# Performance work log

Hardware: AMD Instinct MI355X
Metric: run time of the kernel (lower is better)

The kernel has to match this reference:

```python
import jax, jax.numpy as jnp
import numpy as np

B, CIN, C, N, K = 2, 64, 128, 8192, 16
GROUPS = C // 16
EPS = 1e-5


def lrelu(x):
    return jnp.where(x >= 0, x, 0.1 * x)


def conv1d(x, w, b):  # x:(B,Ci,N) w:(Co,Ci)
    return jnp.einsum('oc,bcn->bon', w, x) + b[None, :, None]


def conv2d(x, w, b):  # x:(B,Ci,N,K) w:(Co,Ci)
    return jnp.einsum('oc,bcnk->bonk', w, x) + b[None, :, None, None]


def groupnorm(x, gamma, beta, groups=GROUPS):
    # normalize over (C/groups, *spatial) per sample per group
    b, c = x.shape[0], x.shape[1]
    xr = x.reshape(b, groups, -1)
    mean = xr.mean(-1, keepdims=True)
    var = xr.var(-1, keepdims=True)
    xn = ((xr - mean) * jax.lax.rsqrt(var + EPS)).reshape(x.shape)
    shp = (1, c) + (1,) * (x.ndim - 2)
    return xn * gamma.reshape(shp) + beta.reshape(shp)


def knn_idx(xyz, k):  # xyz:(B,3,N) -> idx:(B,N,K)
    pts = jnp.transpose(xyz, (0, 2, 1))  # (B,N,3)
    sq = jnp.sum(pts * pts, axis=-1)  # (B,N)
    inner = jnp.einsum('bnc,bmc->bnm', pts, pts)
    d2 = sq[:, :, None] + sq[:, None, :] - 2.0 * inner  # (B,N,N)
    _, idx = jax.lax.top_k(-d2, k)
    return idx


def group(x, idx):  # x:(B,C,N) idx:(B,N,K) -> (B,C,N,K)
    b, c, n = x.shape
    k = idx.shape[-1]
    idxe = jnp.broadcast_to(idx.reshape(b, 1, n * k), (b, c, n * k))
    return jnp.take_along_axis(x, idxe, axis=2).reshape(b, c, n, k)


def reference(xyz, feat, pre_w, pre_b, wq_w, wq_b, wk_w, wk_b, wv_w, wv_b,
              pos1_w, pos1_b, pos1_g, pos1_be, pos2_w, pos2_b,
              att1_w, att1_b, att1_g, att1_be, att2_w, att2_b,
              post_w, post_b, post_g, post_be):
    idx = knn_idx(xyz, K)  # (B,N,K)
    new_feat = conv1d(feat, pre_w, pre_b)  # (B,C,N)
    rel = group(xyz, idx) - xyz[:, :, :, None]  # (B,3,N,K)
    pos = lrelu(groupnorm(conv2d(rel, pos1_w, pos1_b), pos1_g, pos1_be))
    pos = conv2d(pos, pos2_w, pos2_b)  # (B,C,N,K)
    q = conv1d(new_feat, wq_w, wq_b)
    k = group(conv1d(new_feat, wk_w, wk_b), idx)  # (B,C,N,K)
    v = group(conv1d(new_feat, wv_w, wv_b), idx)
    att = q[:, :, :, None] - k + pos
    att = lrelu(groupnorm(conv2d(att, att1_w, att1_b), att1_g, att1_be))
    att = conv2d(att, att2_w, att2_b)
    att = jax.nn.softmax(att, axis=3)
    out = jnp.sum(att * v, axis=3)  # (B,C,N)
    out = lrelu(groupnorm(conv1d(out + new_feat, post_w, post_b), post_g, post_be))
    return out


def setup_inputs():
    key = jax.random.key(0)
    ks = jax.random.split(key, 16)
    s = 0.05
    d = {
        'xyz': jax.random.normal(ks[0], (B, 3, N), jnp.float32),
        'feat': jax.random.normal(ks[1], (B, CIN, N), jnp.float32),
        'pre_w': jax.random.normal(ks[2], (C, CIN), jnp.float32) * s,
        'pre_b': jnp.zeros((C,), jnp.float32),
        'wq_w': jax.random.normal(ks[3], (C, C), jnp.float32) * s,
        'wq_b': jnp.zeros((C,), jnp.float32),
        'wk_w': jax.random.normal(ks[4], (C, C), jnp.float32) * s,
        'wk_b': jnp.zeros((C,), jnp.float32),
        'wv_w': jax.random.normal(ks[5], (C, C), jnp.float32) * s,
        'wv_b': jnp.zeros((C,), jnp.float32),
        'pos1_w': jax.random.normal(ks[6], (C, 3), jnp.float32) * s,
        'pos1_b': jnp.zeros((C,), jnp.float32),
        'pos1_g': jnp.ones((C,), jnp.float32),
        'pos1_be': jnp.zeros((C,), jnp.float32),
        'pos2_w': jax.random.normal(ks[7], (C, C), jnp.float32) * s,
        'pos2_b': jnp.zeros((C,), jnp.float32),
        'att1_w': jax.random.normal(ks[8], (C, C), jnp.float32) * s,
        'att1_b': jnp.zeros((C,), jnp.float32),
        'att1_g': jnp.ones((C,), jnp.float32),
        'att1_be': jnp.zeros((C,), jnp.float32),
        'att2_w': jax.random.normal(ks[9], (C, C), jnp.float32) * s,
        'att2_b': jnp.zeros((C,), jnp.float32),
        'post_w': jax.random.normal(ks[10], (C, C), jnp.float32) * s,
        'post_b': jnp.zeros((C,), jnp.float32),
        'post_g': jnp.ones((C,), jnp.float32),
        'post_be': jnp.zeros((C,), jnp.float32),
    }
    return d
```

## Files before the change

### kernel.cpp

```cpp
#include <hip/hip_runtime.h>
#include <hip/hip_bf16.h>

#define BB 2
#define NN 8192
#define CC 128
#define CIN_ 64
#define KK 16
#define EPSV 1e-5f

typedef __attribute__((ext_vector_type(8))) short short8;
typedef __attribute__((ext_vector_type(4))) float f32x4;

static const size_t OFF_NF   = 262144;
static const size_t OFF_OUT2 = OFF_NF  + 2097152;
static const size_t OFF_Y    = OFF_OUT2 + 2097152;
static const size_t OFF_AQB  = OFF_Y   + 16777216;
static const size_t OFF_AKB  = OFF_AQB + 1048576;
static const size_t OFF_VFB  = OFF_AKB + 1048576;
static const size_t OFF_WQ2  = OFF_VFB + 1048576;
static const size_t OFF_WK2  = OFF_WQ2 + 16384;
static const size_t OFF_PWT  = OFF_WK2 + 16384;
static const size_t OFF_W2B  = OFF_PWT + 16384;
static const size_t OFF_A2B  = OFF_W2B + 8192;
static const size_t OFF_BY   = OFF_A2B + 8192;
static const size_t OFF_RST  = OFF_BY  + 128;
static const size_t OFF_REDA = OFF_RST + 32;
static const size_t OFF_REDP = OFF_REDA + 32;
static const size_t OFF_S1   = OFF_REDP + 32;
static const size_t OFF_T1   = OFF_S1 + 256;
static const size_t OFF_S2   = OFF_T1 + 256;
static const size_t OFF_T2   = OFF_S2 + 256;
static const size_t OFF_S3   = OFF_T2 + 256;
static const size_t OFF_T3   = OFF_S3 + 256;
static const size_t OFF_PTS4 = OFF_T3 + 256;
static const size_t OFF_PTA  = OFF_PTS4 + 65536;
static const size_t OFF_PTP  = OFF_PTA + 65536;

__device__ __forceinline__ unsigned fkey_u(float d) {
  unsigned u = __float_as_uint(d);
  return (u & 0x80000000u) ? ~u : (u | 0x80000000u);
}
__device__ __forceinline__ unsigned long long shflx64(unsigned long long v, int m) {
  int lo = __shfl_xor((int)(unsigned)(v & 0xffffffffu), m, 64);
  int hi = __shfl_xor((int)(unsigned)(v >> 32), m, 64);
  return ((unsigned long long)(unsigned)hi << 32) | (unsigned)lo;
}
__device__ __forceinline__ float bf2f(unsigned short u) {
  return __uint_as_float((unsigned)u << 16);
}
__device__ __forceinline__ unsigned short f2bf(float f) {
  __hip_bfloat16 h = __float2bfloat16(f);
  unsigned short r;
  __builtin_memcpy(&r, &h, 2);
  return r;
}
__device__ __forceinline__ unsigned pack2bf(float a, float b) {
  return (unsigned)f2bf(a) | ((unsigned)f2bf(b) << 16);
}

__global__ __launch_bounds__(128) void prep_weights(
    const float* __restrict__ att1_w, const float* __restrict__ wq_w, const float* __restrict__ wk_w,
    const float* __restrict__ pos2_w, const float* __restrict__ att2_w, const float* __restrict__ post_w,
    const float* __restrict__ wq_b, const float* __restrict__ wk_b, const float* __restrict__ pos2_b,
    const float* __restrict__ att1_b,
    float* __restrict__ WQ2, float* __restrict__ WK2, __hip_bfloat16* __restrict__ W2b,
    __hip_bfloat16* __restrict__ A2b, float* __restrict__ PWT, float* __restrict__ bias_y) {
  int blk = blockIdx.x, t = threadIdx.x;
  if (blk < 128) {
    int c = blk;
    __shared__ float row[128];
    row[t] = att1_w[c * 128 + t];
    __syncthreads();
    float sq = 0.f, sk = 0.f, sp = 0.f;
    for (int m = 0; m < 128; ++m) {
      float r = row[m];
      sq = fmaf(r, wq_w[m * 128 + t], sq);
      sk = fmaf(r, wk_w[m * 128 + t], sk);
      sp = fmaf(r, pos2_w[m * 128 + t], sp);
    }
    WQ2[c * 128 + t] = sq;
    WK2[c * 128 + t] = sk;
    W2b[c * 128 + t] = __float2bfloat16(sp);
  } else if (blk == 128) {
    for (int e = t; e < 16384; e += 128) {
      int c = e >> 7, cp = e & 127;
      A2b[e] = __float2bfloat16(att2_w[e]);
      PWT[cp * 128 + c] = post_w[e];
    }
  } else {
    float s = att1_b[t];
    for (int m = 0; m < 128; ++m)
      s = fmaf(att1_w[t * 128 + m], wq_b[m] - wk_b[m] + pos2_b[m], s);
    bias_y[t] = s;
  }
}

__global__ __launch_bounds__(256) void pts4_kernel(const float* __restrict__ xyz,
                                                   float4* __restrict__ pts4) {
  int e = blockIdx.x * 256 + threadIdx.x;
  int b = e >> 13, n = e & 8191;
  const float* X = xyz + b * 3 * NN;
  float x = X[n], y = X[NN + n], z = X[2 * NN + n];
  pts4[e] = make_float4(-2.0f * x, -2.0f * y, -2.0f * z, fmaf(z, z, fmaf(y, y, x * x)));
}

#define SLOTS 96
__global__ __launch_bounds__(512) void knn_kernel(const float4* __restrict__ pts4,
                                                  int* __restrict__ idxb) {
  __shared__ float4 tile[2048];
  __shared__ unsigned long long list[32][SLOTS];
  __shared__ float chm[32][33];
  __shared__ int cnt[32];
  int t = threadIdx.x;
  int wid = t >> 6, lane = t & 63;
  int q = lane & 31, sub = lane >> 5;
  int blk = blockIdx.x;
  int b = blk >> 8;
  int q0 = (blk & 255) << 5;
  const float4* P = pts4 + b * NN;
  float4 qv = P[q0 + q];
  float qx = -0.5f * qv.x, qy = -0.5f * qv.y, qz = -0.5f * qv.z;
  if (t < 32) cnt[t] = 0;
  int tbase = (wid << 8) + (sub << 7);

  {
    float4 r0 = P[t], r1 = P[512 + t], r2 = P[1024 + t], r3 = P[1536 + t];
    tile[t] = r0; tile[512 + t] = r1; tile[1024 + t] = r2; tile[1536 + t] = r3;
  }
  __syncthreads();
  for (int s = 0; s < 4; ++s) {
    float4 p0, p1, p2, p3;
    if (s < 3) {
      const float4* S = P + ((s + 1) << 11);
      p0 = S[t]; p1 = S[512 + t]; p2 = S[1024 + t]; p3 = S[1536 + t];
    }
    const float4* T = &tile[tbase];
    float mm = 3.4e38f;
    for (int i = 0; i < 128; i += 8) {
      float d[8];
#pragma unroll
      for (int u = 0; u < 8; ++u) {
        float4 cv = T[i + u];
        d[u] = fmaf(qx, cv.x, fmaf(qy, cv.y, fmaf(qz, cv.z, cv.w)));
      }
      mm = fminf(mm, fminf(fminf(fminf(d[0], d[1]), fminf(d[2], d[3])),
                           fminf(fminf(d[4], d[5]), fminf(d[6], d[7]))));
    }
    mm = fminf(mm, __shfl_xor(mm, 32));
    __syncthreads();
    if (s < 3) {
      tile[t] = p0; tile[512 + t] = p1; tile[1024 + t] = p2; tile[1536 + t] = p3;
    }
    if (lane < 32) chm[lane][(s << 3) + wid] = mm;
    __syncthreads();
  }

  float tau;
  {
    float v[32];
#pragma unroll
    for (int i = 0; i < 32; ++i) v[i] = chm[q][i];
    float lo = v[0], hi = v[0];
#pragma unroll
    for (int i = 1; i < 32; ++i) { lo = fminf(lo, v[i]); hi = fmaxf(hi, v[i]); }
    for (int it = 0; it < 12; ++it) {
      float mid = 0.5f * (lo + hi);
      int c = 0;
#pragma unroll
      for (int i = 0; i < 32; ++i) c += (v[i] <= mid) ? 1 : 0;
      if (c >= 16) hi = mid; else lo = mid;
    }
    tau = hi;
  }

  {
    float4 r0 = P[t], r1 = P[512 + t], r2 = P[1024 + t], r3 = P[1536 + t];
    __syncthreads();
    tile[t] = r0; tile[512 + t] = r1; tile[1024 + t] = r2; tile[1536 + t] = r3;
  }
  __syncthreads();
  for (int s = 0; s < 4; ++s) {
    float4 p0, p1, p2, p3;
    if (s < 3) {
      const float4* S = P + ((s + 1) << 11);
      p0 = S[t]; p1 = S[512 + t]; p2 = S[1024 + t]; p3 = S[1536 + t];
    }
    const float4* T = &tile[tbase];
    int gbase = (s << 11) + tbase;
    for (int i = 0; i < 128; i += 4) {
      float d[4];
#pragma unroll
      for (int u = 0; u < 4; ++u) {
        float4 cv = T[i + u];
        d[u] = fmaf(qx, cv.x, fmaf(qy, cv.y, fmaf(qz, cv.z, cv.w)));
      }
#pragma unroll
      for (int u = 0; u < 4; ++u) {
        if (d[u] <= tau) {
          int sl = atomicAdd(&cnt[q], 1);
          if (sl < SLOTS)
            list[q][sl] = ((unsigned long long)fkey_u(d[u]) << 32) | (unsigned)(gbase + i + u);
        }
      }
    }
    __syncthreads();
    if (s < 3) {
      tile[t] = p0; tile[512 + t] = p1; tile[1024 + t] = p2; tile[1536 + t] = p3;
    }
    __syncthreads();
  }

  for (int pp = 0; pp < 2; ++pp) {
    int qa = (wid << 2) + pp * 2, qb2 = qa + 1;
    int ca = cnt[qa]; if (ca > SLOTS) ca = SLOTS;
    int cb3 = cnt[qb2]; if (cb3 > SLOTS) cb3 = SLOTS;
    unsigned long long k0a = (lane < ca) ? list[qa][lane] : ~0ULL;
    unsigned long long k1a = (lane + 64 < ca) ? list[qa][lane + 64] : ~0ULL;
    unsigned long long k0b = (lane < cb3) ? list[qb2][lane] : ~0ULL;
    unsigned long long k1b = (lane + 64 < cb3) ? list[qb2][lane + 64] : ~0ULL;
    for (int r = 0; r < 16; ++r) {
      unsigned long long wa = (k0a < k1a) ? k0a : k1a;
      unsigned long long wb = (k0b < k1b) ? k0b : k1b;
      for (int off = 32; off; off >>= 1) {
        unsigned long long oa = shflx64(wa, off);
        unsigned long long ob = shflx64(wb, off);
        if (oa < wa) wa = oa;
        if (ob < wb) wb = ob;
      }
      if (k0a == wa) k0a = ~0ULL; else if (k1a == wa) k1a = ~0ULL;
      if (k0b == wb) k0b = ~0ULL; else if (k1b == wb) k1b = ~0ULL;
      if (lane == 0) {
        idxb[((size_t)(b * NN) + q0 + qa) * 16 + r] = (int)(wa & 0xffffffffu);
        idxb[((size_t)(b * NN) + q0 + qb2) * 16 + r] = (int)(wb & 0xffffffffu);
      }
    }
  }
}

__global__ __launch_bounds__(256) void relstats_kernel(const float* __restrict__ xyz,
                                                       const int* __restrict__ idxb,
                                                       float* __restrict__ rst) {
  int b = blockIdx.x >> 8;
  int nbase = (blockIdx.x & 255) << 5;
  const float* X = xyz + b * 3 * NN;
  float a[9];
#pragma unroll
  for (int m = 0; m < 9; ++m) a[m] = 0.f;
  for (int e = threadIdx.x; e < 512; e += 256) {
    int nn = nbase + (e >> 4);
    int kk = e & 15;
    int j = idxb[(b * NN + nn) * 16 + kk];
    float rx = X[j] - X[nn];
    float ry = X[NN + j] - X[NN + nn];
    float rz = X[2 * NN + j] - X[2 * NN + nn];
    a[0] += rx; a[1] += ry; a[2] += rz;
    a[3] = fmaf(rx, rx, a[3]); a[4] = fmaf(rx, ry, a[4]); a[5] = fmaf(rx, rz, a[5]);
    a[6] = fmaf(ry, ry, a[6]); a[7] = fmaf(ry, rz, a[7]); a[8] = fmaf(rz, rz, a[8]);
  }
  __shared__ float red[4][9];
  int lane = threadIdx.x & 63, wid = threadIdx.x >> 6;
#pragma unroll
  for (int m = 0; m < 9; ++m) {
    float v = a[m];
    for (int off = 32; off; off >>= 1) v += __shfl_xor(v, off, 64);
    if (lane == 0) red[wid][m] = v;
  }
  __syncthreads();
  if (threadIdx.x < 9) {
    float v = red[0][threadIdx.x] + red[1][threadIdx.x] + red[2][threadIdx.x] + red[3][threadIdx.x];
    atomicAdd(&rst[b * 16 + threadIdx.x], v);
  }
}

__global__ __launch_bounds__(256) void t1_kernel(const float* __restrict__ rst,
    const float* __restrict__ pos1_w, const float* __restrict__ pos1_b,
    const float* __restrict__ pos1_g, const float* __restrict__ pos1_be,
    float* __restrict__ s1, float* __restrict__ t1) {
  __shared__ float gsum[16], gsum2[16];
  int t = threadIdx.x;
  if (t < 16) { gsum[t] = 0.f; gsum2[t] = 0.f; }
  __syncthreads();
  int b = t >> 7, c = t & 127;
  const float* S = rst + b * 16;
  const float Minv = 1.0f / (float)(NN * KK);
  float mx = S[0] * Minv, my = S[1] * Minv, mz = S[2] * Minv;
  float Mxx = S[3] * Minv, Mxy = S[4] * Minv, Mxz = S[5] * Minv;
  float Myy = S[6] * Minv, Myz = S[7] * Minv, Mzz = S[8] * Minv;
  float w0 = pos1_w[c * 3], w1 = pos1_w[c * 3 + 1], w2 = pos1_w[c * 3 + 2];
  float bb = pos1_b[c];
  float wm = w0 * mx + w1 * my + w2 * mz;
  float Ey = wm + bb;
  float q = w0 * w0 * Mxx + w1 * w1 * Myy + w2 * w2 * Mzz
          + 2.f * (w0 * w1 * Mxy + w0 * w2 * Mxz + w1 * w2 * Myz);
  float Ey2 = q + 2.f * bb * wm + bb * bb;
  int g = c >> 4;
  atomicAdd(&gsum[b * 8 + g], Ey);
  atomicAdd(&gsum2[b * 8 + g], Ey2);
  __syncthreads();
  float mean = gsum[b * 8 + g] * (1.f / 16.f);
  float var = fmaxf(gsum2[b * 8 + g] * (1.f / 16.f) - mean * mean, 0.f);
  float r = rsqrtf(var + EPSV);
  float sv = pos1_g[c] * r;
  s1[t] = sv;
  t1[t] = fmaf(sv, bb, pos1_be[c] - mean * sv);
}

__global__ __launch_bounds__(256) void feat_kernel(
    const float* __restrict__ feat, const float* __restrict__ pre_w, const float* __restrict__ pre_b,
    const float* __restrict__ WQ2, const float* __restrict__ WK2,
    const float* __restrict__ wv_w, const float* __restrict__ wv_b,
    float* __restrict__ nf, __hip_bfloat16* __restrict__ AqTb,
    __hip_bfloat16* __restrict__ AkTb, __hip_bfloat16* __restrict__ vfTb) {
  int b = blockIdx.x >> 9;
  int n0 = (blockIdx.x & 511) << 4;
  __shared__ float fe[64][20];
  __shared__ float nfs[128][20];
  int t = threadIdx.x;
  for (int e = t; e < 1024; e += 256) {
    int ci = e >> 4, nn2 = e & 15;
    fe[ci][nn2] = feat[(b * 64 + ci) * NN + n0 + nn2];
  }
  __syncthreads();
  int nq = t & 3, cw = t >> 2;
  {
    float acc[2][4];
#pragma unroll
    for (int m = 0; m < 2; ++m) {
      float bv = pre_b[cw + 64 * m];
      acc[m][0] = bv; acc[m][1] = bv; acc[m][2] = bv; acc[m][3] = bv;
    }
    for (int i = 0; i < 64; ++i) {
      float4 x = *(const float4*)&fe[i][nq << 2];
      float w0 = pre_w[cw * 64 + i];
      float w1 = pre_w[(cw + 64) * 64 + i];
      acc[0][0] = fmaf(w0, x.x, acc[0][0]); acc[0][1] = fmaf(w0, x.y, acc[0][1]);
      acc[0][2] = fmaf(w0, x.z, acc[0][2]); acc[0][3] = fmaf(w0, x.w, acc[0][3]);
      acc[1][0] = fmaf(w1, x.x, acc[1][0]); acc[1][1] = fmaf(w1, x.y, acc[1][1]);
      acc[1][2] = fmaf(w1, x.z, acc[1][2]); acc[1][3] = fmaf(w1, x.w, acc[1][3]);
    }
#pragma unroll
    for (int m = 0; m < 2; ++m) {
      int c = cw + 64 * m;
      float4 v = make_float4(acc[m][0], acc[m][1], acc[m][2], acc[m][3]);
      *(float4*)&nfs[c][nq << 2] = v;
      *(float4*)&nf[(b * 128 + c) * NN + n0 + (nq << 2)] = v;
    }
  }
  __syncthreads();
  for (int s = 0; s < 3; ++s) {
    const float* Wm = (s == 0) ? WQ2 : ((s == 1) ? WK2 : wv_w);
    __hip_bfloat16* D = (s == 0) ? AqTb : ((s == 1) ? AkTb : vfTb);
    float acc[2][4];
#pragma unroll
    for (int m = 0; m < 2; ++m) {
      float bv = (s == 2) ? wv_b[cw + 64 * m] : 0.f;
      acc[m][0] = bv; acc[m][1] = bv; acc[m][2] = bv; acc[m][3] = bv;
    }
    for (int i = 0; i < 128; ++i) {
      float4 x = *(const float4*)&nfs[i][nq << 2];
      float w0 = Wm[cw * 128 + i];
      float w1 = Wm[(cw + 64) * 128 + i];
      acc[0][0] = fmaf(w0, x.x, acc[0][0]); acc[0][1] = fmaf(w0, x.y, acc[0][1]);
      acc[0][2] = fmaf(w0, x.z, acc[0][2]); acc[0][3] = fmaf(w0, x.w, acc[0][3]);
      acc[1][0] = fmaf(w1, x.x, acc[1][0]); acc[1][1] = fmaf(w1, x.y, acc[1][1]);
      acc[1][2] = fmaf(w1, x.z, acc[1][2]); acc[1][3] = fmaf(w1, x.w, acc[1][3]);
    }
#pragma unroll
    for (int m = 0; m < 2; ++m) {
      int c = cw + 64 * m;
#pragma unroll
      for (int v = 0; v < 4; ++v)
        D[(size_t)(b * NN + n0 + (nq << 2) + v) * 128 + c] = __float2bfloat16(acc[m][v]);
    }
  }
}

__global__ __launch_bounds__(256) void y_kernel_mfma(const float* __restrict__ xyz,
    const int* __restrict__ idxb, const __hip_bfloat16* __restrict__ AqTb,
    const __hip_bfloat16* __restrict__ AkTb, const __hip_bfloat16* __restrict__ W2b,
    const float* __restrict__ bias_y, const float* __restrict__ pos1_w,
    const float* __restrict__ s1, const float* __restrict__ t1,
    __hip_bfloat16* __restrict__ ybuf, float* __restrict__ partA) {
  int b = blockIdx.x >> 11;
  int pb = (blockIdx.x & 2047) * 4;
  __shared__ __align__(16) __hip_bfloat16 z_s[64][136];
  __shared__ __align__(16) __hip_bfloat16 ak_s[64][136];
  __shared__ __align__(16) float aq_s[4][128];
  __shared__ float rel_s[64][4];
  __shared__ int jj[64];
  __shared__ float gns[8], gns2[8];
  int t = threadIdx.x;
  int lane = t & 63, wid = t >> 6;
  int l15 = lane & 15, quad = lane >> 4;
  if (t < 8) { gns[t] = 0.f; gns2[t] = 0.f; }
  if (t < 64) {
    int n = pb + (t >> 4);
    int j = idxb[(b * NN + pb) * 16 + t];
    jj[t] = j;
    const float* X = xyz + b * 3 * NN;
    rel_s[t][0] = X[j] - X[n];
    rel_s[t][1] = X[NN + j] - X[NN + n];
    rel_s[t][2] = X[2 * NN + j] - X[2 * NN + n];
  }
  for (int e = t; e < 512; e += 256) {
    int pt = e >> 7, c = e & 127;
    aq_s[pt][c] = bf2f(((const unsigned short*)AqTb)[((size_t)(b * NN) + pb + pt) * 128 + c]) + bias_y[c];
  }
  __syncthreads();
  {
    int cpp = t & 63, pg = t >> 6;
    int cp0 = cpp * 2;
    float w00 = pos1_w[cp0 * 3], w01 = pos1_w[cp0 * 3 + 1], w02 = pos1_w[cp0 * 3 + 2];
    float w10 = pos1_w[cp0 * 3 + 3], w11 = pos1_w[cp0 * 3 + 4], w12 = pos1_w[cp0 * 3 + 5];
    float sa = s1[b * 128 + cp0], ta = t1[b * 128 + cp0];
    float sb = s1[b * 128 + cp0 + 1], tb = t1[b * 128 + cp0 + 1];
#pragma unroll
    for (int i = 0; i < 16; ++i) {
      int pix = pg * 16 + i;
      float rx = rel_s[pix][0], ry = rel_s[pix][1], rz = rel_s[pix][2];
      float u0 = fmaf(w02, rz, fmaf(w01, ry, w00 * rx));
      float u1 = fmaf(w12, rz, fmaf(w11, ry, w10 * rx));
      float z0 = fmaf(sa, u0, ta); z0 = (z0 >= 0.f) ? z0 : 0.1f * z0;
      float z1 = fmaf(sb, u1, tb); z1 = (z1 >= 0.f) ? z1 : 0.1f * z1;
      *(unsigned*)&z_s[pix][cp0] = pack2bf(z0, z1);
    }
  }
  for (int e = t; e < 4096; e += 256) {
    int pix = e >> 6, cpp = e & 63;
    *(unsigned*)&ak_s[pix][cpp * 2] =
        *(const unsigned*)((const unsigned short*)AkTb + ((size_t)(b * NN) + jj[pix]) * 128 + cpp * 2);
  }
  short8 afr[2][4];
#pragma unroll
  for (int m2 = 0; m2 < 2; ++m2) {
    int row = (wid * 2 + m2) * 16 + l15;
#pragma unroll
    for (int k0 = 0; k0 < 4; ++k0)
      afr[m2][k0] = *(const short8*)((const unsigned short*)W2b + row * 128 + k0 * 32 + quad * 8);
  }
  __syncthreads();
  f32x4 acc[2][4];
#pragma unroll
  for (int m2 = 0; m2 < 2; ++m2)
#pragma unroll
    for (int nt = 0; nt < 4; ++nt) acc[m2][nt] = (f32x4){0.f, 0.f, 0.f, 0.f};
#pragma unroll
  for (int k0 = 0; k0 < 4; ++k0) {
#pragma unroll
    for (int nt = 0; nt < 4; ++nt) {
      short8 bfr = *(const short8*)&z_s[nt * 16 + l15][k0 * 32 + quad * 8];
      acc[0][nt] = __builtin_amdgcn_mfma_f32_16x16x32_bf16(afr[0][k0], bfr, acc[0][nt], 0, 0, 0);
      acc[1][nt] = __builtin_amdgcn_mfma_f32_16x16x32_bf16(afr[1][k0], bfr, acc[1][nt], 0, 0, 0);
    }
  }
  float lsum[2] = {0.f, 0.f}, lsum2[2] = {0.f, 0.f};
#pragma unroll
  for (int m2 = 0; m2 < 2; ++m2) {
    int c0 = (wid * 2 + m2) * 16 + quad * 4;
#pragma unroll
    for (int nt = 0; nt < 4; ++nt) {
      int pix = nt * 16 + l15;
      ushort4 au = *(ushort4*)&ak_s[pix][c0];
      float4 aq = *(float4*)&aq_s[nt][c0];
      f32x4 a = acc[m2][nt];
      float v0 = a[0] + aq.x - bf2f(au.x);
      float v1 = a[1] + aq.y - bf2f(au.y);
      float v2 = a[2] + aq.z - bf2f(au.z);
      float v3 = a[3] + aq.w - bf2f(au.w);
      lsum[m2] += (v0 + v1) + (v2 + v3);
      lsum2[m2] += fmaf(v0, v0, fmaf(v1, v1, fmaf(v2, v2, v3 * v3)));
      ushort4 yo;
      yo.x = f2bf(v0); yo.y = f2bf(v1); yo.z = f2bf(v2); yo.w = f2bf(v3);
      *(ushort4*)&ak_s[pix][c0] = yo;
    }
  }
#pragma unroll
  for (int m2 = 0; m2 < 2; ++m2) {
    float s = lsum[m2], s2 = lsum2[m2];
    for (int msk = 1; msk < 64; msk <<= 1) {
      s += __shfl_xor(s, msk);
      s2 += __shfl_xor(s2, msk);
    }
    if (lane == 0) {
      atomicAdd(&gns[wid * 2 + m2], s);
      atomicAdd(&gns2[wid * 2 + m2], s2);
    }
  }
  __syncthreads();
  size_t ybase = ((size_t)(b * NN) + pb) * 16;
  unsigned short* yb = (unsigned short*)ybuf;
  for (int e = t; e < 4096; e += 256) {
    int pix = e >> 6, cpp = e & 63;
    *(unsigned*)(yb + (ybase + pix) * 128 + cpp * 2) = *(unsigned*)&ak_s[pix][cpp * 2];
  }
  if (t < 8) {
    partA[(size_t)t * 4096 + blockIdx.x] = gns[t];
    partA[(size_t)(8 + t) * 4096 + blockIdx.x] = gns2[t];
  }
}

__global__ __launch_bounds__(256) void gnred_kernel(const float* __restrict__ part,
                                                    float* __restrict__ red) {
  int k = blockIdx.x;
  int pb = k >> 4, idx = k & 15;
  const float* p = part + (size_t)idx * 4096 + pb * 2048;
  float s = 0.f;
  for (int i = threadIdx.x; i < 2048; i += 256) s += p[i];
  __shared__ float rs[4];
  int lane = threadIdx.x & 63, wid = threadIdx.x >> 6;
  for (int off = 32; off; off >>= 1) s += __shfl_xor(s, off);
  if (lane == 0) rs[wid] = s;
  __syncthreads();
  if (threadIdx.x == 0) red[k] = rs[0] + rs[1] + rs[2] + rs[3];
}

__global__ __launch_bounds__(256) void gnaff_kernel(const float* __restrict__ red,
    const float* __restrict__ gamma, const float* __restrict__ beta, float Minv,
    float* __restrict__ sarr, float* __restrict__ tarr) {
  int t = threadIdx.x;
  int b = t >> 7, c = t & 127, g = c >> 4;
  float S = red[b * 16 + g], S2 = red[b * 16 + 8 + g];
  float mean = S * Minv;
  float var = fmaxf(S2 * Minv - mean * mean, 0.f);
  float r = rsqrtf(var + EPSV);
  float sv = gamma[c] * r;
  sarr[t] = sv;
  tarr[t] = beta[c] - mean * sv;
}

__global__ __launch_bounds__(256) void att_out_kernel(const __hip_bfloat16* __restrict__ ybuf,
    const int* __restrict__ idxb, const float* __restrict__ s2, const float* __restrict__ t2,
    const __hip_bfloat16* __restrict__ A2b, const __hip_bfloat16* __restrict__ vfTb,
    const float* __restrict__ nf, const float* __restrict__ PWT, const float* __restrict__ post_b,
    float* __restrict__ out2, float* __restrict__ partP) {
  int b = blockIdx.x >> 11;
  int pb = (blockIdx.x & 2047) * 4;
  __shared__ __align__(16) __hip_bfloat16 h_s[64][136];
  __shared__ __align__(16) __hip_bfloat16 v_s[64][136];
  __shared__ __align__(16) float opre[4][132];
  __shared__ int jj[64];
  __shared__ float gns[8], gns2[8];
  int t = threadIdx.x;
  int lane = t & 63, wid = t >> 6;
  int l15 = lane & 15, quad = lane >> 4;
  if (t < 8) { gns[t] = 0.f; gns2[t] = 0.f; }
  if (t < 64) jj[t] = idxb[(b * NN + pb) * 16 + t];
  __syncthreads();
  size_t ybase = ((size_t)(b * NN) + pb) * 16;
  const unsigned short* yb = (const unsigned short*)ybuf;
  {
    int cpp = t & 63, pg = t >> 6;
    int c0 = cpp * 2;
    float sa = s2[b * 128 + c0], ta = t2[b * 128 + c0];
    float sb = s2[b * 128 + c0 + 1], tb = t2[b * 128 + c0 + 1];
#pragma unroll
    for (int i = 0; i < 16; ++i) {
      int pix = pg * 16 + i;
      unsigned u = *(const unsigned*)(yb + (ybase + pix) * 128 + c0);
      float y0 = bf2f((unsigned short)(u & 0xffff));
      float y1 = bf2f((unsigned short)(u >> 16));
      float h0 = fmaf(sa, y0, ta); h0 = (h0 >= 0.f) ? h0 : 0.1f * h0;
      float h1 = fmaf(sb, y1, tb); h1 = (h1 >= 0.f) ? h1 : 0.1f * h1;
      *(unsigned*)&h_s[pix][c0] = pack2bf(h0, h1);
    }
  }
  for (int e = t; e < 4096; e += 256) {
    int pix = e >> 6, cpp = e & 63;
    *(unsigned*)&v_s[pix][cpp * 2] =
        *(const unsigned*)((const unsigned short*)vfTb + ((size_t)(b * NN) + jj[pix]) * 128 + cpp * 2);
  }
  short8 afr[2][4];
#pragma unroll
  for (int m2 = 0; m2 < 2; ++m2) {
    int row = (wid * 2 + m2) * 16 + l15;
#pragma unroll
    for (int k0 = 0; k0 < 4; ++k0)
      afr[m2][k0] = *(const short8*)((const unsigned short*)A2b + row * 128 + k0 * 32 + quad * 8);
  }
  __syncthreads();
  f32x4 acc[2][4];
#pragma unroll
  for (int m2 = 0; m2 < 2; ++m2)
#pragma unroll
    for (int nt = 0; nt < 4; ++nt) acc[m2][nt] = (f32x4){0.f, 0.f, 0.f, 0.f};
#pragma unroll
  for (int k0 = 0; k0 < 4; ++k0) {
#pragma unroll
    for (int nt = 0; nt < 4; ++nt) {
      short8 bfr = *(const short8*)&h_s[nt * 16 + l15][k0 * 32 + quad * 8];
      acc[0][nt] = __builtin_amdgcn_mfma_f32_16x16x32_bf16(afr[0][k0], bfr, acc[0][nt], 0, 0, 0);
      acc[1][nt] = __builtin_amdgcn_mfma_f32_16x16x32_bf16(afr[1][k0], bfr, acc[1][nt], 0, 0, 0);
    }
  }
#pragma unroll
  for (int m2 = 0; m2 < 2; ++m2) {
    int c0 = (wid * 2 + m2) * 16 + quad * 4;
#pragma unroll
    for (int nt = 0; nt < 4; ++nt) {
      f32x4 a = acc[m2][nt];
      float mx[4], ex[4], sm[4], ws[4];
#pragma unroll
      for (int r = 0; r < 4; ++r) mx[r] = a[r];
#pragma unroll
      for (int msk = 1; msk < 16; msk <<= 1)
#pragma unroll
        for (int r = 0; r < 4; ++r) mx[r] = fmaxf(mx[r], __shfl_xor(mx[r], msk));
#pragma unroll
      for (int r = 0; r < 4; ++r) { ex[r] = __expf(a[r] - mx[r]); sm[r] = ex[r]; }
#pragma unroll
      for (int msk = 1; msk < 16; msk <<= 1)
#pragma unroll
        for (int r = 0; r < 4; ++r) sm[r] += __shfl_xor(sm[r], msk);
      ushort4 vu = *(const ushort4*)&v_s[nt * 16 + l15][c0];
      ws[0] = ex[0] * bf2f(vu.x);
      ws[1] = ex[1] * bf2f(vu.y);
      ws[2] = ex[2] * bf2f(vu.z);
      ws[3] = ex[3] * bf2f(vu.w);
#pragma unroll
      for (int msk = 1; msk < 16; msk <<= 1)
#pragma unroll
        for (int r = 0; r < 4; ++r) ws[r] += __shfl_xor(ws[r], msk);
      if (l15 == 0) {
        float4 o;
        o.x = ws[0] / sm[0]; o.y = ws[1] / sm[1];
        o.z = ws[2] / sm[2]; o.w = ws[3] / sm[3];
        *(float4*)&opre[nt][c0] = o;
      }
    }
  }
  __syncthreads();
  {
    int c = t & 127, g = t >> 7;
#pragma unroll
    for (int pp2 = 0; pp2 < 2; ++pp2) {
      int pt = g * 2 + pp2;
      opre[pt][c] += nf[(size_t)(b * 128 + c) * NN + pb + pt];
    }
  }
  __syncthreads();
  {
    int c = t & 127, g = t >> 7;
    float a0 = post_b[c], a1 = a0;
    for (int cp = 0; cp < 128; ++cp) {
      float w = PWT[cp * 128 + c];
      a0 = fmaf(w, opre[g * 2][cp], a0);
      a1 = fmaf(w, opre[g * 2 + 1][cp], a1);
    }
    out2[(size_t)(b * 128 + c) * NN + pb + g * 2] = a0;
    out2[(size_t)(b * 128 + c) * NN + pb + g * 2 + 1] = a1;
    atomicAdd(&gns[c >> 4], a0 + a1);
    atomicAdd(&gns2[c >> 4], fmaf(a0, a0, a1 * a1));
  }
  __syncthreads();
  if (t < 8) {
    partP[(size_t)t * 4096 + blockIdx.x] = gns[t];
    partP[(size_t)(8 + t) * 4096 + blockIdx.x] = gns2[t];
  }
}

__global__ __launch_bounds__(256) void final_kernel(const float* __restrict__ out2,
    const float* __restrict__ s3, const float* __restrict__ t3, float* __restrict__ out) {
  int e = blockIdx.x * 256 + threadIdx.x;
  int c = (e >> 13) & 127, b = e >> 20;
  float v = fmaf(s3[b * 128 + c], out2[e], t3[b * 128 + c]);
  out[e] = (v >= 0.f) ? v : 0.1f * v;
}

extern "C" void kernel_launch(void* const* d_in, const int* in_sizes, int n_in,
                              void* d_out, int out_size, void* d_ws, size_t ws_size,
                              hipStream_t stream) {
  (void)in_sizes; (void)n_in; (void)out_size; (void)ws_size;
  const float* xyz     = (const float*)d_in[0];
  const float* feat    = (const float*)d_in[1];
  const float* pre_w   = (const float*)d_in[2];
  const float* pre_b   = (const float*)d_in[3];
  const float* wq_w    = (const float*)d_in[4];
  const float* wq_b    = (const float*)d_in[5];
  const float* wk_w    = (const float*)d_in[6];
  const float* wk_b    = (const float*)d_in[7];
  const float* wv_w    = (const float*)d_in[8];
  const float* wv_b    = (const float*)d_in[9];
  const float* pos1_w  = (const float*)d_in[10];
  const float* pos1_b  = (const float*)d_in[11];
  const float* pos1_g  = (const float*)d_in[12];
  const float* pos1_be = (const float*)d_in[13];
  const float* pos2_w  = (const float*)d_in[14];
  const float* pos2_b  = (const float*)d_in[15];
  const float* att1_w  = (const float*)d_in[16];
  const float* att1_b  = (const float*)d_in[17];
  const float* att1_g  = (const float*)d_in[18];
  const float* att1_be = (const float*)d_in[19];
  const float* att2_w  = (const float*)d_in[20];
  const float* post_w  = (const float*)d_in[22];
  const float* post_b  = (const float*)d_in[23];
  const float* post_g  = (const float*)d_in[24];
  const float* post_be = (const float*)d_in[25];

  float* W = (float*)d_ws;
  int* idxb = (int*)d_ws;
  float* nf   = W + OFF_NF;
  float* out2 = W + OFF_OUT2;
  __hip_bfloat16* ybuf = (__hip_bfloat16*)(W + OFF_Y);
  __hip_bfloat16* AqTb = (__hip_bfloat16*)(W + OFF_AQB);
  __hip_bfloat16* AkTb = (__hip_bfloat16*)(W + OFF_AKB);
  __hip_bfloat16* vfTb = (__hip_bfloat16*)(W + OFF_VFB);
  float* WQ2  = W + OFF_WQ2;
  float* WK2  = W + OFF_WK2;
  float* PWT  = W + OFF_PWT;
  __hip_bfloat16* W2b = (__hip_bfloat16*)(W + OFF_W2B);
  __hip_bfloat16* A2b = (__hip_bfloat16*)(W + OFF_A2B);
  float* BY   = W + OFF_BY;
  float* RST  = W + OFF_RST;
  float* REDA = W + OFF_REDA;
  float* REDP = W + OFF_REDP;
  float* S1 = W + OFF_S1; float* T1 = W + OFF_T1;
  float* S2 = W + OFF_S2; float* T2 = W + OFF_T2;
  float* S3 = W + OFF_S3; float* T3 = W + OFF_T3;
  float4* PTS4 = (float4*)(W + OFF_PTS4);
  float* PARTA = W + OFF_PTA;
  float* PARTP = W + OFF_PTP;

  hipMemsetAsync(RST, 0, 32 * sizeof(float), stream);

  prep_weights<<<130, 128, 0, stream>>>(att1_w, wq_w, wk_w, pos2_w, att2_w, post_w,
                                        wq_b, wk_b, pos2_b, att1_b,
                                        WQ2, WK2, W2b, A2b, PWT, BY);
  pts4_kernel<<<64, 256, 0, stream>>>(xyz, PTS4);
  knn_kernel<<<512, 512, 0, stream>>>(PTS4, idxb);
  relstats_kernel<<<512, 256, 0, stream>>>(xyz, idxb, RST);
  t1_kernel<<<1, 256, 0, stream>>>(RST, pos1_w, pos1_b, pos1_g, pos1_be, S1, T1);
  feat_kernel<<<1024, 256, 0, stream>>>(feat, pre_w, pre_b, WQ2, WK2, wv_w, wv_b,
                                        nf, AqTb, AkTb, vfTb);
  y_kernel_mfma<<<4096, 256, 0, stream>>>(xyz, idxb, AqTb, AkTb, W2b, BY, pos1_w, S1, T1, ybuf, PARTA);
  gnred_kernel<<<32, 256, 0, stream>>>(PARTA, REDA);
  gnaff_kernel<<<1, 256, 0, stream>>>(REDA, att1_g, att1_be, 1.0f / 2097152.0f, S2, T2);
  att_out_kernel<<<4096, 256, 0, stream>>>(ybuf, idxb, S2, T2, A2b, vfTb, nf, PWT, post_b, out2, PARTP);
  gnred_kernel<<<32, 256, 0, stream>>>(PARTP, REDP);
  gnaff_kernel<<<1, 256, 0, stream>>>(REDP, post_g, post_be, 1.0f / 131072.0f, S3, T3);
  final_kernel<<<8192, 256, 0, stream>>>(out2, S3, T3, (float*)d_out);
}
```

Baseline: 424.8 us.

## Stage attention logits through shared memory for per-thread softmax instead of shuffles

Replaces the cross-lane shuffle reductions for softmax max, sum and weighted-value sum with a transpose of the MFMA accumulators into a shared-memory scratch buffer that reuses the h_s storage. Each thread then owns one (point, channel) row of 16 neighbor logits and does the softmax and value dot product serially. The residual nf add is folded into the same step. This removes the many shfl_xor operations but adds two extra barriers per pass and shared-memory writes and reads with possible bank conflicts.

Measured after the change: 389.7 us. 8.2% less time.

```diff
diff --git a/kernel.cpp b/kernel.cpp
--- a/kernel.cpp
+++ b/kernel.cpp
@@ -535,7 +535,10 @@
     float* __restrict__ out2, float* __restrict__ partP) {
   int b = blockIdx.x >> 11;
   int pb = (blockIdx.x & 2047) * 4;
-  __shared__ __align__(16) __hip_bfloat16 h_s[64][136];
+  __shared__ __align__(16) union HS {
+    unsigned short h[64][136];
+    float sc[2][128][17];
+  } hs;
   __shared__ __align__(16) __hip_bfloat16 v_s[64][136];
   __shared__ __align__(16) float opre[4][132];
   __shared__ int jj[64];
@@ -561,7 +564,7 @@
       float y1 = bf2f((unsigned short)(u >> 16));
       float h0 = fmaf(sa, y0, ta); h0 = (h0 >= 0.f) ? h0 : 0.1f * h0;
       float h1 = fmaf(sb, y1, tb); h1 = (h1 >= 0.f) ? h1 : 0.1f * h1;
-      *(unsigned*)&h_s[pix][c0] = pack2bf(h0, h1);
+      *(unsigned*)&hs.h[pix][c0] = pack2bf(h0, h1);
     }
   }
   for (int e = t; e < 4096; e += 256) {
@@ -587,54 +590,47 @@
   for (int k0 = 0; k0 < 4; ++k0) {
 #pragma unroll
     for (int nt = 0; nt < 4; ++nt) {
-      short8 bfr = *(const short8*)&h_s[nt * 16 + l15][k0 * 32 + quad * 8];
+      short8 bfr = *(const short8*)&hs.h[nt * 16 + l15][k0 * 32 + quad * 8];
       acc[0][nt] = __builtin_amdgcn_mfma_f32_16x16x32_bf16(afr[0][k0], bfr, acc[0][nt], 0, 0, 0);
       acc[1][nt] = __builtin_amdgcn_mfma_f32_16x16x32_bf16(afr[1][k0], bfr, acc[1][nt], 0, 0, 0);
     }
   }
-#pragma unroll
-  for (int m2 = 0; m2 < 2; ++m2) {
-    int c0 = (wid * 2 + m2) * 16 + quad * 4;
-#pragma unroll
-    for (int nt = 0; nt < 4; ++nt) {
-      f32x4 a = acc[m2][nt];
-      float mx[4], ex[4], sm[4], ws[4];
-#pragma unroll
-      for (int r = 0; r < 4; ++r) mx[r] = a[r];
-#pragma unroll
-      for (int msk = 1; msk < 16; msk <<= 1)
-#pragma unroll
-        for (int r = 0; r < 4; ++r) mx[r] = fmaxf(mx[r], __shfl_xor(mx[r], msk));
-#pragma unroll
-      for (int r = 0; r < 4; ++r) { ex[r] = __expf(a[r] - mx[r]); sm[r] = ex[r]; }
-#pragma unroll
-      for (int msk = 1; msk < 16; msk <<= 1)
-#pragma unroll
-        for (int r = 0; r < 4; ++r) sm[r] += __shfl_xor(sm[r], msk);
-      ushort4 vu = *(const ushort4*)&v_s[nt * 16 + l15][c0];
-      ws[0] = ex[0] * bf2f(vu.x);
-      ws[1] = ex[1] * bf2f(vu.y);
-      ws[2] = ex[2] * bf2f(vu.z);
-      ws[3] = ex[3] * bf2f(vu.w);
-#pragma unroll
-      for (int msk = 1; msk < 16; msk <<= 1)
-#pragma unroll
-        for (int r = 0; r < 4; ++r) ws[r] += __shfl_xor(ws[r], msk);
-      if (l15 == 0) {
-        float4 o;
-        o.x = ws[0] / sm[0]; o.y = ws[1] / sm[1];
-        o.z = ws[2] / sm[2]; o.w = ws[3] / sm[3];
-        *(float4*)&opre[nt][c0] = o;
+  int pidx = t >> 7;
+  int cch = t & 127;
+#pragma unroll
+  for (int pass = 0; pass < 2; ++pass) {
+    __syncthreads();
+#pragma unroll
+    for (int ntl = 0; ntl < 2; ++ntl) {
+      int nt = pass * 2 + ntl;
+#pragma unroll
+      for (int m2 = 0; m2 < 2; ++m2) {
+        int cb = (wid * 2 + m2) * 16 + quad * 4;
+        f32x4 a = acc[m2][nt];
+#pragma unroll
+        for (int r = 0; r < 4; ++r) hs.sc[ntl][cb + r][l15] = a[r];
       }
     }
-  }
-  __syncthreads();
-  {
-    int c = t & 127, g = t >> 7;
-#pragma unroll
-    for (int pp2 = 0; pp2 < 2; ++pp2) {
-      int pt = g * 2 + pp2;
-      opre[pt][c] += nf[(size_t)(b * 128 + c) * NN + pb + pt];
+    __syncthreads();
+    {
+      int p = pass * 2 + pidx;
+      float nfv = nf[(size_t)(b * 128 + cch) * NN + pb + p];
+      const float* srow = hs.sc[pidx][cch];
+      float sv[16];
+#pragma unroll
+      for (int k = 0; k < 16; ++k) sv[k] = srow[k];
+      float mx = sv[0];
+#pragma unroll
+      for (int k = 1; k < 16; ++k) mx = fmaxf(mx, sv[k]);
+      float sm = 0.f, dot = 0.f;
+#pragma unroll
+      for (int k = 0; k < 16; ++k) {
+        float e = __expf(sv[k] - mx);
+        sm += e;
+        float vv = bf2f(*(const unsigned short*)&v_s[p * 16 + k][cch]);
+        dot = fmaf(e, vv, dot);
+      }
+      opre[p][cch] = dot / sm + nfv;
     }
   }
   __syncthreads();
```
